# Kernel optimization log

Hardware: AMD Instinct MI355X
Metric: run time of the kernel (lower is better)

Reference implementation:

```python
import jax, jax.numpy as jnp
import numpy as np

B, F, H, D, TE, CE = 16384, 1024, 64, 256, 4, 4

def setup_inputs() -> dict:
    key = jax.random.key(0)
    ks = iter(jax.random.split(key, 40))
    s = 0.02
    mk = lambda shape: jax.random.normal(next(ks), shape, jnp.float32) * s
    inp = {
        'x_A': jax.random.normal(next(ks), (B, F), jnp.float32),
        'x_S': jax.random.normal(next(ks), (B, F), jnp.float32),
        'x_B': jax.random.normal(next(ks), (B, F), jnp.float32),
        # stacked per-expert weights for the three expert groups (A, Shared, B)
        'W1A': mk((TE, F, H)), 'b1A': mk((TE, H)), 'W2A': mk((TE, H, D)), 'b2A': mk((TE, D)),
        'W1S': mk((CE, F, H)), 'b1S': mk((CE, H)), 'W2S': mk((CE, H, D)), 'b2S': mk((CE, D)),
        'W1B': mk((TE, F, H)), 'b1B': mk((TE, H)), 'W2B': mk((TE, H, D)), 'b2B': mk((TE, D)),
        # gate weights
        'WgA': mk((F, TE + CE)), 'bgA': mk((TE + CE,)),
        'WgB': mk((F, TE + CE)), 'bgB': mk((TE + CE,)),
        'WgS': mk((F, 2 * TE + CE)), 'bgS': mk((2 * TE + CE,)),
    }
    return inp

def _expert_group(x, W1, b1, W2, b2):
    # x: [B,F], W1: [E,F,H] -> [B,E,H]; W2: [E,H,D] -> [B,E,D]
    h = jax.nn.relu(jnp.einsum('bf,efh->beh', x, W1) + b1)  # dropout p=0 -> identity
    return jax.nn.relu(jnp.einsum('beh,ehd->bed', h, W2) + b2)

def reference(x_A, x_S, x_B,
              W1A, b1A, W2A, b2A,
              W1S, b1S, W2S, b2S,
              W1B, b1B, W2B, b2B,
              WgA, bgA, WgB, bgB, WgS, bgS):
    EA = _expert_group(x_A, W1A, b1A, W2A, b2A)  # [B,TE,D]
    ES = _expert_group(x_S, W1S, b1S, W2S, b2S)  # [B,CE,D]
    EB = _expert_group(x_B, W1B, b1B, W2B, b2B)  # [B,TE,D]
    gA = jax.nn.softmax(x_A @ WgA + bgA, axis=1)  # [B,TE+CE]
    gS = jax.nn.softmax(x_S @ WgS + bgS, axis=1)  # [B,2TE+CE]
    gB = jax.nn.softmax(x_B @ WgB + bgB, axis=1)  # [B,TE+CE]
    outA = jnp.einsum('bed,be->bd', jnp.concatenate([EA, ES], axis=1), gA)
    outS = jnp.einsum('bed,be->bd', jnp.concatenate([EA, ES, EB], axis=1), gS)
    outB = jnp.einsum('bed,be->bd', jnp.concatenate([EB, ES], axis=1), gB)
    return (outA, outS, outB)
```

## Files before the change

kernel.cpp:

```cpp
#include <hip/hip_runtime.h>


#define BB 16384
#define FF 1024

typedef _Float16 f16;
typedef __fp16 h16x2 __attribute__((ext_vector_type(2)));
typedef _Float16 f16x8 __attribute__((ext_vector_type(8)));
typedef float f32x4 __attribute__((ext_vector_type(4)));

__device__ __forceinline__ void load_lds16(const void* g, void* l) {
    __builtin_amdgcn_global_load_lds(
        (const __attribute__((address_space(1))) unsigned int*)g,
        (__attribute__((address_space(3))) unsigned int*)l, 16, 0, 0);
}

__device__ __forceinline__ f16x8 pack8(float4 lo, float4 hi) {
    union { f16x8 v; h16x2 p[4]; } u;
    u.p[0] = __builtin_amdgcn_cvt_pkrtz(lo.x, lo.y);
    u.p[1] = __builtin_amdgcn_cvt_pkrtz(lo.z, lo.w);
    u.p[2] = __builtin_amdgcn_cvt_pkrtz(hi.x, hi.y);
    u.p[3] = __builtin_amdgcn_cvt_pkrtz(hi.z, hi.w);
    return u.v;
}

__global__ __launch_bounds__(256) void pack_kernel(
    const float* __restrict__ W1A, const float* __restrict__ W1S, const float* __restrict__ W1B,
    const float* __restrict__ W2A, const float* __restrict__ W2S, const float* __restrict__ W2B,
    const float* __restrict__ WgA, const float* __restrict__ WgS, const float* __restrict__ WgB,
    f16* __restrict__ Wp, f16* __restrict__ W2T, f16* __restrict__ Gp)
{
    int idx = blockIdx.x * 256 + threadIdx.x;
    if (idx < 786432) {
        int g = idx / 262144, rem = idx % 262144;
        int c = rem >> 10, k = rem & 1023;
        const float* W1 = (g == 0) ? W1A : ((g == 1) ? W1S : W1B);
        Wp[idx] = (f16)W1[((c >> 6) << 16) + k * 64 + (c & 63)];
    } else if (idx < 983040) {
        int j = idx - 786432;
        int g = j / 65536, rem = j % 65536;
        int e = rem >> 14, rr = rem & 16383;
        int d = rr >> 6, hh = rr & 63;
        const float* W2 = (g == 0) ? W2A : ((g == 1) ? W2S : W2B);
        W2T[j] = (f16)W2[e * 16384 + hh * 256 + d];
    } else {
        int j = idx - 983040;
        int g = j / 16384, rem = j % 16384;
        int k = rem >> 4, c = rem & 15;
        int ng = (g == 1) ? 12 : 8;
        const float* Wg = (g == 0) ? WgA : ((g == 1) ? WgS : WgB);
        Gp[j] = (c < ng) ? (f16)Wg[k * ng + c] : (f16)0.0f;
    }
}

__global__ __launch_bounds__(256) void l1_kernel(
    const float* __restrict__ xA, const float* __restrict__ xS, const float* __restrict__ xB,
    const float* __restrict__ b1A, const float* __restrict__ b1S, const float* __restrict__ b1B,
    const float* __restrict__ bgA, const float* __restrict__ bgS, const float* __restrict__ bgB,
    const f16* __restrict__ Wp,
    const f16* __restrict__ Gp,
    f16* __restrict__ hbuf,
    float* __restrict__ gates)
{
    const int g = blockIdx.z;
    const float* x  = (g == 0) ? xA  : ((g == 1) ? xS  : xB);
    const float* b1 = (g == 0) ? b1A : ((g == 1) ? b1S : b1B);
    const float* bg = (g == 0) ? bgA : ((g == 1) ? bgS : bgB);
    const int ng = (g == 1) ? 12 : 8;
    float* gout = gates + ((g == 0) ? (size_t)0
                         : (g == 1) ? (size_t)BB * 8
                                    : (size_t)BB * 8 + (size_t)BB * 12);

    const int row0 = blockIdx.y * 128;
    const int col0 = blockIdx.x * 128;
    const bool do_gate = (blockIdx.x == 0);

    __shared__ __align__(16) float Asf[128 * 32];
    __shared__ __align__(16) f16   Bsh[128 * 32];
    __shared__ __align__(16) f16   Gs[16 * 40];

    const int tid  = threadIdx.x;
    const int lane = tid & 63;
    const int wave = tid >> 6;
    const int wm = (wave >> 1) * 64;
    const int wn = (wave & 1) * 64;
    const int lrow = lane & 15;
    const int quad = lane >> 4;

    const f16* Wgrp = Wp + (size_t)g * 256 * 1024;
    const f16* Ggrp = Gp + (size_t)g * 1024 * 16;

    f32x4 acc[4][4] = {};
    f32x4 gacc[4] = {};
    const bool my_gate = do_gate && ((wave & 1) == 0);

    for (int k0 = 0; k0 < FF; k0 += 32) {
#pragma unroll
        for (int r = 0; r < 4; ++r) {
            int s = r * 256 + tid;
            int m = s >> 3, slot = s & 7;
            int seg = slot ^ (m & 7);
            load_lds16(x + (size_t)(row0 + m) * FF + k0 + seg * 4, Asf + s * 4);
        }
#pragma unroll
        for (int r = 0; r < 2; ++r) {
            int s = r * 256 + tid;
            int m = s >> 2, slot = s & 3;
            int seg = slot ^ ((m >> 1) & 3);
            load_lds16(Wgrp + (size_t)(col0 + m) * FF + k0 + seg * 8, Bsh + s * 8);
        }
        if (do_gate) {
#pragma unroll
            for (int r = 0; r < 2; ++r) {
                int idx = r * 256 + tid;
                int k = idx >> 4, c = idx & 15;
                Gs[c * 40 + k] = Ggrp[(size_t)(k0 + k) * 16 + c];
            }
        }
        __syncthreads();

        f16x8 af[4], bfr[4];
#pragma unroll
        for (int i = 0; i < 4; ++i) {
            int m = wm + i * 16 + lrow;
            const float* rp = Asf + m * 32;
            int s0 = (2 * quad) ^ (m & 7);
            int s1 = s0 ^ 1;
            float4 lo = *(const float4*)(rp + s0 * 4);
            float4 hi = *(const float4*)(rp + s1 * 4);
            af[i] = pack8(lo, hi);
        }
#pragma unroll
        for (int j = 0; j < 4; ++j) {
            int n = wn + j * 16 + lrow;
            int slot = quad ^ ((n >> 1) & 3);
            bfr[j] = *(const f16x8*)(Bsh + n * 32 + slot * 8);
        }
#pragma unroll
        for (int i = 0; i < 4; ++i)
#pragma unroll
            for (int j = 0; j < 4; ++j)
                acc[i][j] = __builtin_amdgcn_mfma_f32_16x16x32_f16(af[i], bfr[j], acc[i][j], 0, 0, 0);
        if (my_gate) {
            f16x8 gb = *(const f16x8*)(Gs + lrow * 40 + quad * 8);
#pragma unroll
            for (int i = 0; i < 4; ++i)
                gacc[i] = __builtin_amdgcn_mfma_f32_16x16x32_f16(af[i], gb, gacc[i], 0, 0, 0);
        }
        __syncthreads();
    }

#pragma unroll
    for (int j = 0; j < 4; ++j) {
        int c = col0 + wn + j * 16 + lrow;
        float bias = b1[c];
#pragma unroll
        for (int i = 0; i < 4; ++i) {
#pragma unroll
            for (int r = 0; r < 4; ++r) {
                int row = row0 + wm + i * 16 + quad * 4 + r;
                float v = fmaxf(acc[i][j][r] + bias, 0.0f);
                hbuf[((size_t)g * BB + row) * 256 + c] = (f16)v;
            }
        }
    }

    if (my_gate) {
        int c = lrow;
        bool valid = (c < ng);
        float bias = valid ? bg[c] : 0.0f;
#pragma unroll
        for (int i = 0; i < 4; ++i) {
#pragma unroll
            for (int r = 0; r < 4; ++r) {
                int row = row0 + wm + i * 16 + quad * 4 + r;
                float logit = valid ? (gacc[i][r] + bias) : -1e30f;
                float mx = logit;
#pragma unroll
                for (int m = 1; m < 16; m <<= 1)
                    mx = fmaxf(mx, __shfl_xor(mx, m, 16));
                float ev = valid ? __expf(logit - mx) : 0.0f;
                float sum = ev;
#pragma unroll
                for (int m = 1; m < 16; m <<= 1)
                    sum += __shfl_xor(sum, m, 16);
                if (valid) gout[(size_t)row * ng + c] = ev / sum;
            }
        }
    }
}

__global__ __launch_bounds__(256) void l2_kernel(
    const f16* __restrict__ hbuf,
    const f16* __restrict__ W2T,
    const float* __restrict__ b2A, const float* __restrict__ b2S, const float* __restrict__ b2B,
    const float* __restrict__ gates,
    float* __restrict__ out)
{
    const int o = blockIdx.y;
    const int row0 = blockIdx.x * 64;
    const int tid = threadIdx.x;
    const int lane = tid & 63;
    const int wave = tid >> 6;
    const int wn = wave * 64;
    const int lrow = lane & 15;
    const int quad = lane >> 4;

    const int ng = (o == 1) ? 12 : 8;
    const float* gp = gates + ((o == 0) ? (size_t)0
                             : (o == 1) ? (size_t)BB * 8
                                        : (size_t)BB * 8 + (size_t)BB * 12);

    __shared__ __align__(16) f16 Ash[64 * 64];
    __shared__ __align__(16) f16 Bsh[256 * 64];
    __shared__ float gsh[64 * 12];

    for (int idx = tid; idx < 64 * ng; idx += 256)
        gsh[idx] = gp[(size_t)(row0 + idx / ng) * ng + (idx % ng)];

    f32x4 oacc[4][4] = {};
    const int nc = ng;

    for (int k = 0; k < nc; ++k) {
        int e = k & 3, gc = k, gi;
        if (o == 0)      gi = (k < 4) ? 0 : 1;
        else if (o == 1) gi = k >> 2;
        else             gi = (k < 4) ? 2 : 1;

        const f16* hs = hbuf + ((size_t)gi * BB + row0) * 256 + e * 64;
        const f16* w2 = W2T + (size_t)(gi * 4 + e) * 256 * 64;
        const float* b2 = (gi == 0) ? b2A : ((gi == 1) ? b2S : b2B);

        __syncthreads();
#pragma unroll
        for (int r = 0; r < 2; ++r) {
            int s = r * 256 + tid;
            int m = s >> 3, slot = s & 7;
            int seg = slot ^ (m & 7);
            load_lds16(hs + (size_t)m * 256 + seg * 8, Ash + s * 8);
        }
#pragma unroll
        for (int r = 0; r < 8; ++r) {
            int s = r * 256 + tid;
            int m = s >> 3, slot = s & 7;
            int seg = slot ^ (m & 7);
            load_lds16(w2 + (size_t)m * 64 + seg * 8, Bsh + s * 8);
        }
        __syncthreads();

        f32x4 eacc[4][4] = {};
#pragma unroll
        for (int kk = 0; kk < 2; ++kk) {
            f16x8 af[4], bfr[4];
#pragma unroll
            for (int i = 0; i < 4; ++i) {
                int rr = i * 16 + lrow;
                int slot = (kk * 4 + quad) ^ (rr & 7);
                af[i] = *(const f16x8*)(Ash + rr * 64 + slot * 8);
            }
#pragma unroll
            for (int j = 0; j < 4; ++j) {
                int n = wn + j * 16 + lrow;
                int slot = (kk * 4 + quad) ^ (n & 7);
                bfr[j] = *(const f16x8*)(Bsh + n * 64 + slot * 8);
            }
#pragma unroll
            for (int i = 0; i < 4; ++i)
#pragma unroll
                for (int j = 0; j < 4; ++j)
                    eacc[i][j] = __builtin_amdgcn_mfma_f32_16x16x32_f16(af[i], bfr[j], eacc[i][j], 0, 0, 0);
        }

#pragma unroll
        for (int j = 0; j < 4; ++j) {
            int d = wn + j * 16 + lrow;
            float bias = b2[e * 256 + d];
#pragma unroll
            for (int i = 0; i < 4; ++i) {
#pragma unroll
                for (int r = 0; r < 4; ++r) {
                    int rl = i * 16 + quad * 4 + r;
                    float v = fmaxf(eacc[i][j][r] + bias, 0.0f);
                    oacc[i][j][r] += gsh[rl * ng + gc] * v;
                }
            }
        }
    }

#pragma unroll
    for (int j = 0; j < 4; ++j) {
        int d = wn + j * 16 + lrow;
#pragma unroll
        for (int i = 0; i < 4; ++i) {
#pragma unroll
            for (int r = 0; r < 4; ++r) {
                int rl = i * 16 + quad * 4 + r;
                out[((size_t)o * BB + row0 + rl) * 256 + d] = oacc[i][j][r];
            }
        }
    }
}

extern "C" void kernel_launch(void* const* d_in, const int* in_sizes, int n_in,
                              void* d_out, int out_size, void* d_ws, size_t ws_size,
                              hipStream_t stream)
{
    (void)in_sizes; (void)n_in; (void)out_size; (void)ws_size;

    const float* xA  = (const float*)d_in[0];
    const float* xS  = (const float*)d_in[1];
    const float* xB  = (const float*)d_in[2];
    const float* W1A = (const float*)d_in[3];
    const float* b1A = (const float*)d_in[4];
    const float* W2A = (const float*)d_in[5];
    const float* b2A = (const float*)d_in[6];
    const float* W1S = (const float*)d_in[7];
    const float* b1S = (const float*)d_in[8];
    const float* W2S = (const float*)d_in[9];
    const float* b2S = (const float*)d_in[10];
    const float* W1B = (const float*)d_in[11];
    const float* b1B = (const float*)d_in[12];
    const float* W2B = (const float*)d_in[13];
    const float* b2B = (const float*)d_in[14];
    const float* WgA = (const float*)d_in[15];
    const float* bgA = (const float*)d_in[16];
    const float* WgB = (const float*)d_in[17];
    const float* bgB = (const float*)d_in[18];
    const float* WgS = (const float*)d_in[19];
    const float* bgS = (const float*)d_in[20];

    char* ws = (char*)d_ws;
    f16*   Wp   = (f16*)(ws);
    f16*   W2T  = (f16*)(ws + 0x180000);
    f16*   Gp   = (f16*)(ws + 0x1E0000);
    f16*   hbuf = (f16*)(ws + 0x200000);
    float* gate = (float*)(ws + 0x200000 + 0x1800000);

    pack_kernel<<<4032, 256, 0, stream>>>(W1A, W1S, W1B, W2A, W2S, W2B,
                                          WgA, WgS, WgB, Wp, W2T, Gp);
    l1_kernel<<<dim3(2, 128, 3), 256, 0, stream>>>(
        xA, xS, xB, b1A, b1S, b1B, bgA, bgS, bgB,
        Wp, Gp, hbuf, gate);
    l2_kernel<<<dim3(256, 3), 256, 0, stream>>>(
        hbuf, W2T, b2A, b2S, b2B, gate, (float*)d_out);
}
```

Baseline: 336.5 us.

## Widen L1 tiles to full hidden width, double-buffer LDS, drop LDS in L2

L1 now uses 512-thread blocks that each cover all 256 hidden columns for 128 rows. Each x tile is therefore read once instead of twice, and the gate computation runs in every block. LDS loads are double-buffered with one barrier per k-step, and gate weights are repacked so they can be read directly from global memory into registers. L2 moves to 512 threads and loads hidden activations and W2 fragments straight from global memory with no LDS staging or per-expert barriers. The risks are fewer L1 blocks (384) on a large GPU and uncoalesced global fragment loads in L2.

```diff
diff --git a/kernel.cpp b/kernel.cpp
--- a/kernel.cpp
+++ b/kernel.cpp
@@ -28,7 +28,7 @@
     const float* __restrict__ W1A, const float* __restrict__ W1S, const float* __restrict__ W1B,
     const float* __restrict__ W2A, const float* __restrict__ W2S, const float* __restrict__ W2B,
     const float* __restrict__ WgA, const float* __restrict__ WgS, const float* __restrict__ WgB,
-    f16* __restrict__ Wp, f16* __restrict__ W2T, f16* __restrict__ Gp)
+    f16* __restrict__ Wp, f16* __restrict__ W2T, f16* __restrict__ Gp2)
 {
     int idx = blockIdx.x * 256 + threadIdx.x;
     if (idx < 786432) {
@@ -46,23 +46,23 @@
     } else {
         int j = idx - 983040;
         int g = j / 16384, rem = j % 16384;
-        int k = rem >> 4, c = rem & 15;
+        int c = rem >> 10, k = rem & 1023;
         int ng = (g == 1) ? 12 : 8;
         const float* Wg = (g == 0) ? WgA : ((g == 1) ? WgS : WgB);
-        Gp[j] = (c < ng) ? (f16)Wg[k * ng + c] : (f16)0.0f;
-    }
-}
-
-__global__ __launch_bounds__(256) void l1_kernel(
+        Gp2[j] = (c < ng) ? (f16)Wg[k * ng + c] : (f16)0.0f;
+    }
+}
+
+__global__ __launch_bounds__(512, 4) void l1_kernel(
     const float* __restrict__ xA, const float* __restrict__ xS, const float* __restrict__ xB,
     const float* __restrict__ b1A, const float* __restrict__ b1S, const float* __restrict__ b1B,
     const float* __restrict__ bgA, const float* __restrict__ bgS, const float* __restrict__ bgB,
     const f16* __restrict__ Wp,
-    const f16* __restrict__ Gp,
+    const f16* __restrict__ Gp2,
     f16* __restrict__ hbuf,
     float* __restrict__ gates)
 {
-    const int g = blockIdx.z;
+    const int g = blockIdx.y;
     const float* x  = (g == 0) ? xA  : ((g == 1) ? xS  : xB);
     const float* b1 = (g == 0) ? b1A : ((g == 1) ? b1S : b1B);
     const float* bg = (g == 0) ? bgA : ((g == 1) ? bgS : bgB);
@@ -71,88 +71,96 @@
                          : (g == 1) ? (size_t)BB * 8
                                     : (size_t)BB * 8 + (size_t)BB * 12);
 
-    const int row0 = blockIdx.y * 128;
-    const int col0 = blockIdx.x * 128;
-    const bool do_gate = (blockIdx.x == 0);
-
-    __shared__ __align__(16) float Asf[128 * 32];
-    __shared__ __align__(16) f16   Bsh[128 * 32];
-    __shared__ __align__(16) f16   Gs[16 * 40];
+    const int row0 = blockIdx.x * 128;
+
+    __shared__ __align__(16) float Asf[2][128 * 32];
+    __shared__ __align__(16) f16   Bsh[2][256 * 32];
 
     const int tid  = threadIdx.x;
     const int lane = tid & 63;
     const int wave = tid >> 6;
-    const int wm = (wave >> 1) * 64;
-    const int wn = (wave & 1) * 64;
+    const int wm = (wave >> 2) * 64;
+    const int wn = (wave & 3) * 64;
     const int lrow = lane & 15;
     const int quad = lane >> 4;
+    const bool my_gate = ((wave & 3) == 0);
 
     const f16* Wgrp = Wp + (size_t)g * 256 * 1024;
-    const f16* Ggrp = Gp + (size_t)g * 1024 * 16;
+    const f16* Ggrp = Gp2 + ((size_t)g * 16 + lrow) * 1024 + quad * 8;
+    const float* xrow = x + (size_t)row0 * FF;
 
     f32x4 acc[4][4] = {};
     f32x4 gacc[4] = {};
-    const bool my_gate = do_gate && ((wave & 1) == 0);
-
+
+#pragma unroll
+    for (int r = 0; r < 2; ++r) {
+        int s = r * 512 + tid;
+        int m = s >> 3, slot = s & 7;
+        int seg = slot ^ (m & 7);
+        load_lds16(xrow + (size_t)m * FF + seg * 4, &Asf[0][s * 4]);
+    }
+#pragma unroll
+    for (int r = 0; r < 2; ++r) {
+        int s = r * 512 + tid;
+        int n = s >> 2, slot = s & 3;
+        int seg = slot ^ ((n >> 1) & 3);
+        load_lds16(Wgrp + (size_t)n * FF + seg * 8, &Bsh[0][s * 8]);
+    }
+
+    int cur = 0;
     for (int k0 = 0; k0 < FF; k0 += 32) {
-#pragma unroll
-        for (int r = 0; r < 4; ++r) {
-            int s = r * 256 + tid;
-            int m = s >> 3, slot = s & 7;
-            int seg = slot ^ (m & 7);
-            load_lds16(x + (size_t)(row0 + m) * FF + k0 + seg * 4, Asf + s * 4);
-        }
-#pragma unroll
-        for (int r = 0; r < 2; ++r) {
-            int s = r * 256 + tid;
-            int m = s >> 2, slot = s & 3;
-            int seg = slot ^ ((m >> 1) & 3);
-            load_lds16(Wgrp + (size_t)(col0 + m) * FF + k0 + seg * 8, Bsh + s * 8);
-        }
-        if (do_gate) {
+        __syncthreads();
+        int nxt = cur ^ 1;
+        if (k0 + 32 < FF) {
 #pragma unroll
             for (int r = 0; r < 2; ++r) {
-                int idx = r * 256 + tid;
-                int k = idx >> 4, c = idx & 15;
-                Gs[c * 40 + k] = Ggrp[(size_t)(k0 + k) * 16 + c];
-            }
-        }
-        __syncthreads();
-
-        f16x8 af[4], bfr[4];
+                int s = r * 512 + tid;
+                int m = s >> 3, slot = s & 7;
+                int seg = slot ^ (m & 7);
+                load_lds16(xrow + (size_t)m * FF + (k0 + 32) + seg * 4, &Asf[nxt][s * 4]);
+            }
+#pragma unroll
+            for (int r = 0; r < 2; ++r) {
+                int s = r * 512 + tid;
+                int n = s >> 2, slot = s & 3;
+                int seg = slot ^ ((n >> 1) & 3);
+                load_lds16(Wgrp + (size_t)n * FF + (k0 + 32) + seg * 8, &Bsh[nxt][s * 8]);
+            }
+        }
+
+        f16x8 gb;
+        if (my_gate) gb = *(const f16x8*)(Ggrp + k0);
+
+        f16x8 af[4];
 #pragma unroll
         for (int i = 0; i < 4; ++i) {
             int m = wm + i * 16 + lrow;
-            const float* rp = Asf + m * 32;
+            const float* rp = &Asf[cur][m * 32];
             int s0 = (2 * quad) ^ (m & 7);
-            int s1 = s0 ^ 1;
             float4 lo = *(const float4*)(rp + s0 * 4);
-            float4 hi = *(const float4*)(rp + s1 * 4);
+            float4 hi = *(const float4*)(rp + (s0 ^ 1) * 4);
             af[i] = pack8(lo, hi);
         }
 #pragma unroll
         for (int j = 0; j < 4; ++j) {
             int n = wn + j * 16 + lrow;
             int slot = quad ^ ((n >> 1) & 3);
-            bfr[j] = *(const f16x8*)(Bsh + n * 32 + slot * 8);
-        }
-#pragma unroll
-        for (int i = 0; i < 4; ++i)
-#pragma unroll
-            for (int j = 0; j < 4; ++j)
-                acc[i][j] = __builtin_amdgcn_mfma_f32_16x16x32_f16(af[i], bfr[j], acc[i][j], 0, 0, 0);
+            f16x8 bf = *(const f16x8*)(&Bsh[cur][n * 32 + slot * 8]);
+#pragma unroll
+            for (int i = 0; i < 4; ++i)
+                acc[i][j] = __builtin_amdgcn_mfma_f32_16x16x32_f16(af[i], bf, acc[i][j], 0, 0, 0);
+        }
         if (my_gate) {
-            f16x8 gb = *(const f16x8*)(Gs + lrow * 40 + quad * 8);
 #pragma unroll
             for (int i = 0; i < 4; ++i)
                 gacc[i] = __builtin_amdgcn_mfma_f32_16x16x32_f16(af[i], gb, gacc[i], 0, 0, 0);
         }
-        __syncthreads();
+        cur = nxt;
     }
 
 #pragma unroll
     for (int j = 0; j < 4; ++j) {
-        int c = col0 + wn + j * 16 + lrow;
+        int c = wn + j * 16 + lrow;
         float bias = b1[c];
 #pragma unroll
         for (int i = 0; i < 4; ++i) {
@@ -190,7 +198,7 @@
     }
 }
 
-__global__ __launch_bounds__(256) void l2_kernel(
+__global__ __launch_bounds__(512) void l2_kernel(
     const f16* __restrict__ hbuf,
     const f16* __restrict__ W2T,
     const float* __restrict__ b2A, const float* __restrict__ b2S, const float* __restrict__ b2B,
@@ -202,7 +210,8 @@
     const int tid = threadIdx.x;
     const int lane = tid & 63;
     const int wave = tid >> 6;
-    const int wn = wave * 64;
+    const int wm = (wave >> 2) * 32;
+    const int wn = (wave & 3) * 64;
     const int lrow = lane & 15;
     const int quad = lane >> 4;
 
@@ -211,77 +220,46 @@
                              : (o == 1) ? (size_t)BB * 8
                                         : (size_t)BB * 8 + (size_t)BB * 12);
 
-    __shared__ __align__(16) f16 Ash[64 * 64];
-    __shared__ __align__(16) f16 Bsh[256 * 64];
     __shared__ float gsh[64 * 12];
-
-    for (int idx = tid; idx < 64 * ng; idx += 256)
+    for (int idx = tid; idx < 64 * ng; idx += 512)
         gsh[idx] = gp[(size_t)(row0 + idx / ng) * ng + (idx % ng)];
-
-    f32x4 oacc[4][4] = {};
-    const int nc = ng;
-
-    for (int k = 0; k < nc; ++k) {
-        int e = k & 3, gc = k, gi;
+    __syncthreads();
+
+    f32x4 oacc[2][4] = {};
+
+    for (int k = 0; k < ng; ++k) {
+        int e = k & 3, gi;
         if (o == 0)      gi = (k < 4) ? 0 : 1;
         else if (o == 1) gi = k >> 2;
         else             gi = (k < 4) ? 2 : 1;
 
-        const f16* hs = hbuf + ((size_t)gi * BB + row0) * 256 + e * 64;
+        const f16* hs = hbuf + ((size_t)gi * BB + row0 + wm) * 256 + e * 64;
         const f16* w2 = W2T + (size_t)(gi * 4 + e) * 256 * 64;
         const float* b2 = (gi == 0) ? b2A : ((gi == 1) ? b2S : b2B);
 
-        __syncthreads();
-#pragma unroll
-        for (int r = 0; r < 2; ++r) {
-            int s = r * 256 + tid;
-            int m = s >> 3, slot = s & 7;
-            int seg = slot ^ (m & 7);
-            load_lds16(hs + (size_t)m * 256 + seg * 8, Ash + s * 8);
-        }
-#pragma unroll
-        for (int r = 0; r < 8; ++r) {
-            int s = r * 256 + tid;
-            int m = s >> 3, slot = s & 7;
-            int seg = slot ^ (m & 7);
-            load_lds16(w2 + (size_t)m * 64 + seg * 8, Bsh + s * 8);
-        }
-        __syncthreads();
-
-        f32x4 eacc[4][4] = {};
-#pragma unroll
-        for (int kk = 0; kk < 2; ++kk) {
-            f16x8 af[4], bfr[4];
-#pragma unroll
-            for (int i = 0; i < 4; ++i) {
-                int rr = i * 16 + lrow;
-                int slot = (kk * 4 + quad) ^ (rr & 7);
-                af[i] = *(const f16x8*)(Ash + rr * 64 + slot * 8);
-            }
-#pragma unroll
-            for (int j = 0; j < 4; ++j) {
-                int n = wn + j * 16 + lrow;
-                int slot = (kk * 4 + quad) ^ (n & 7);
-                bfr[j] = *(const f16x8*)(Bsh + n * 64 + slot * 8);
-            }
-#pragma unroll
-            for (int i = 0; i < 4; ++i)
-#pragma unroll
-                for (int j = 0; j < 4; ++j)
-                    eacc[i][j] = __builtin_amdgcn_mfma_f32_16x16x32_f16(af[i], bfr[j], eacc[i][j], 0, 0, 0);
-        }
+        f16x8 af[2][2];
+#pragma unroll
+        for (int i = 0; i < 2; ++i)
+#pragma unroll
+            for (int kk = 0; kk < 2; ++kk)
+                af[i][kk] = *(const f16x8*)(hs + (size_t)(i * 16 + lrow) * 256 + kk * 32 + quad * 8);
 
 #pragma unroll
         for (int j = 0; j < 4; ++j) {
             int d = wn + j * 16 + lrow;
+            f16x8 bf0 = *(const f16x8*)(w2 + (size_t)d * 64 + quad * 8);
+            f16x8 bf1 = *(const f16x8*)(w2 + (size_t)d * 64 + 32 + quad * 8);
             float bias = b2[e * 256 + d];
 #pragma unroll
-            for (int i = 0; i < 4; ++i) {
+            for (int i = 0; i < 2; ++i) {
+                f32x4 t = {};
+                t = __builtin_amdgcn_mfma_f32_16x16x32_f16(af[i][0], bf0, t, 0, 0, 0);
+                t = __builtin_amdgcn_mfma_f32_16x16x32_f16(af[i][1], bf1, t, 0, 0, 0);
 #pragma unroll
                 for (int r = 0; r < 4; ++r) {
-                    int rl = i * 16 + quad * 4 + r;
-                    float v = fmaxf(eacc[i][j][r] + bias, 0.0f);
-                    oacc[i][j][r] += gsh[rl * ng + gc] * v;
+                    int rl = wm + i * 16 + quad * 4 + r;
+                    float v = fmaxf(t[r] + bias, 0.0f);
+                    oacc[i][j][r] += gsh[rl * ng + k] * v;
                 }
             }
         }
@@ -291,10 +269,10 @@
     for (int j = 0; j < 4; ++j) {
         int d = wn + j * 16 + lrow;
 #pragma unroll
-        for (int i = 0; i < 4; ++i) {
+        for (int i = 0; i < 2; ++i) {
 #pragma unroll
             for (int r = 0; r < 4; ++r) {
-                int rl = i * 16 + quad * 4 + r;
+                int rl = wm + i * 16 + quad * 4 + r;
                 out[((size_t)o * BB + row0 + rl) * 256 + d] = oacc[i][j][r];
             }
         }
@@ -332,15 +310,15 @@
     char* ws = (char*)d_ws;
     f16*   Wp   = (f16*)(ws);
     f16*   W2T  = (f16*)(ws + 0x180000);
-    f16*   Gp   = (f16*)(ws + 0x1E0000);
+    f16*   Gp2  = (f16*)(ws + 0x1E0000);
     f16*   hbuf = (f16*)(ws + 0x200000);
     float* gate = (float*)(ws + 0x200000 + 0x1800000);
 
     pack_kernel<<<4032, 256, 0, stream>>>(W1A, W1S, W1B, W2A, W2S, W2B,
-                                          WgA, WgS, WgB, Wp, W2T, Gp);
-    l1_kernel<<<dim3(2, 128, 3), 256, 0, stream>>>(
+                                          WgA, WgS, WgB, Wp, W2T, Gp2);
+    l1_kernel<<<dim3(128, 3), 512, 0, stream>>>(
         xA, xS, xB, b1A, b1S, b1B, bgA, bgS, bgB,
-        Wp, Gp, hbuf, gate);
-    l2_kernel<<<dim3(256, 3), 256, 0, stream>>>(
+        Wp, Gp2, hbuf, gate);
+    l2_kernel<<<dim3(256, 3), 512, 0, stream>>>(
         hbuf, W2T, b2A, b2S, b2B, gate, (float*)d_out);
 }
```

New measurement: 366.8 us. +9.0%, slower.
